# Optimization experiments

Measured on AMD Instinct MI355X. Metric: run time of the kernel, lower is better.

Reference implementation:

```python
import jax, jax.numpy as jnp
import numpy as np

N_EMBD = 1024
N_HEAD = 16
HEAD_DIM = N_EMBD // N_HEAD


def setup_inputs() -> dict:
    key = jax.random.key(0)
    kx, kq, kk, kv, ko = jax.random.split(key, 5)
    B, S = 2, 2048
    return {
        "x": jax.random.normal(kx, (B, S, N_EMBD), dtype=jnp.float32),
        "W_q": jax.random.normal(kq, (N_EMBD, N_EMBD), dtype=jnp.float32),
        "W_k": jax.random.normal(kk, (N_EMBD, N_EMBD), dtype=jnp.float32),
        "W_v": jax.random.normal(kv, (N_EMBD, N_EMBD), dtype=jnp.float32),
        "W_o": jax.random.normal(ko, (N_EMBD, N_EMBD), dtype=jnp.float32),
    }


def reference(x, W_q, W_k, W_v, W_o):
    B, S, E = x.shape
    H, D = N_HEAD, HEAD_DIM
    scale = 1.0 / np.sqrt(D).astype(np.float32)
    # QKV projections, split into heads: (B, H, S, D)
    q = (x @ W_q).reshape(B, S, H, D).transpose(0, 2, 1, 3)
    k = (x @ W_k).reshape(B, S, H, D).transpose(0, 2, 1, 3)
    v = (x @ W_v).reshape(B, S, H, D).transpose(0, 2, 1, 3)
    # scaled scores with causal mask
    scores = jnp.einsum("bhqd,bhkd->bhqk", q, k) * scale
    causal = jnp.tril(jnp.ones((S, S), dtype=bool))
    scores = jnp.where(causal, scores, -jnp.inf)
    attn = jax.nn.softmax(scores, axis=-1)
    out = jnp.einsum("bhqk,bhkd->bhqd", attn, v)
    out = out.transpose(0, 2, 1, 3).reshape(B, S, E)
    return out @ W_o
```

## Files before the change

### kernel.cpp

```cpp
#include <hip/hip_runtime.h>
#include <stdint.h>

#define E 1024
#define S 2048
#define NH 16
#define HD 64

typedef _Float16 f16;
typedef _Float16 f16x4 __attribute__((ext_vector_type(4)));
typedef _Float16 f16x8 __attribute__((ext_vector_type(8)));
typedef __fp16 hv4 __attribute__((ext_vector_type(4)));
typedef float f32x4 __attribute__((ext_vector_type(4)));

__device__ __forceinline__ void async16(const void* g, void* l) {
  __builtin_amdgcn_global_load_lds(
      (const __attribute__((address_space(1))) unsigned int*)g,
      (__attribute__((address_space(3))) unsigned int*)l, 16, 0, 0);
}


__global__ __launch_bounds__(256) void cvt_x(const float* __restrict__ x,
                                             f16* __restrict__ xh,
                                             f16* __restrict__ xl) {
  int i = (blockIdx.x * 256 + threadIdx.x) * 4;
  float4 a = *(const float4*)(x + i);
  f16 h0 = (f16)a.x, h1 = (f16)a.y, h2 = (f16)a.z, h3 = (f16)a.w;
  f16x4 hv = {h0, h1, h2, h3};
  f16x4 lv = {(f16)(a.x - (float)h0), (f16)(a.y - (float)h1),
              (f16)(a.z - (float)h2), (f16)(a.w - (float)h3)};
  *(f16x4*)(xh + i) = hv;
  *(f16x4*)(xl + i) = lv;
}

__global__ __launch_bounds__(256) void cvt_w(const float* __restrict__ Wq,
                                             const float* __restrict__ Wk,
                                             const float* __restrict__ Wv,
                                             const float* __restrict__ Wo,
                                             f16* __restrict__ Wh,
                                             f16* __restrict__ Wl) {
  __shared__ float tile[32][33];
  const int z = blockIdx.z;
  const float* W = z == 0 ? Wq : z == 1 ? Wk : z == 2 ? Wv : Wo;
  const int tx = threadIdx.x, ty = threadIdx.y;
  const int x0 = blockIdx.x * 32, y0 = blockIdx.y * 32;
#pragma unroll
  for (int i = 0; i < 4; i++)
    tile[ty + i * 8][tx] = W[(size_t)(y0 + ty + i * 8) * E + x0 + tx];
  __syncthreads();
  f16* outh = Wh + (size_t)z * E * E;
  f16* outl = Wl + (size_t)z * E * E;
#pragma unroll
  for (int i = 0; i < 4; i++) {
    float v = tile[tx][ty + i * 8];
    size_t o = (size_t)(x0 + ty + i * 8) * E + (y0 + tx);
    f16 hi = (f16)v;
    outh[o] = hi;
    if (z < 2) outl[o] = (f16)(v - (float)hi);
  }
}


template <bool SPLIT2>
__device__ __forceinline__ void gemm_mainloop(
    const f16* __restrict__ Ah, const f16* __restrict__ Al,
    const f16* __restrict__ Bh, const f16* __restrict__ Bl, int m0, int n0,
    int K, f16* Ahs, f16* Als, f16* Bhs, f16* Bls, f32x4 acc[4][4]) {
  const int tid = threadIdx.x, lane = tid & 63, wid = tid >> 6;
  const int quad = lane >> 4, c16 = lane & 15;
  const int rA = tid >> 2;
  const int cA = (tid & 3) ^ ((rA >> 1) & 3);
  const size_t gA0 = (size_t)(m0 + rA) * K + cA * 8;
  const size_t gA1 = (size_t)(m0 + 64 + rA) * K + cA * 8;
  const size_t gB0 = (size_t)(n0 + rA) * K + cA * 8;
  const size_t gB1 = (size_t)(n0 + 64 + rA) * K + cA * 8;
  const int l0 = tid * 8, l1 = (256 + tid) * 8;
  int a_off[4], b_off[4];
#pragma unroll
  for (int i = 0; i < 4; i++) {
    int ra = (wid >> 1) * 64 + i * 16 + c16;
    a_off[i] = ra * 32 + ((quad ^ ((ra >> 1) & 3)) << 3);
    int rb = (wid & 1) * 64 + i * 16 + c16;
    b_off[i] = rb * 32 + ((quad ^ ((rb >> 1) & 3)) << 3);
  }
  for (int k0 = 0; k0 < K; k0 += 32) {
    __syncthreads();
    async16(Ah + gA0 + k0, Ahs + l0);
    async16(Ah + gA1 + k0, Ahs + l1);
    async16(Bh + gB0 + k0, Bhs + l0);
    async16(Bh + gB1 + k0, Bhs + l1);
    if constexpr (SPLIT2) {
      async16(Al + gA0 + k0, Als + l0);
      async16(Al + gA1 + k0, Als + l1);
      async16(Bl + gB0 + k0, Bls + l0);
      async16(Bl + gB1 + k0, Bls + l1);
    }
    __syncthreads();
    f16x8 ah[4], bh[4];
#pragma unroll
    for (int i = 0; i < 4; i++) {
      ah[i] = *(const f16x8*)(Ahs + a_off[i]);
      bh[i] = *(const f16x8*)(Bhs + b_off[i]);
    }
    if constexpr (SPLIT2) {
      f16x8 al[4], bl[4];
#pragma unroll
      for (int i = 0; i < 4; i++) {
        al[i] = *(const f16x8*)(Als + a_off[i]);
        bl[i] = *(const f16x8*)(Bls + b_off[i]);
      }
#pragma unroll
      for (int i = 0; i < 4; i++)
#pragma unroll
        for (int j = 0; j < 4; j++) {
          acc[i][j] = __builtin_amdgcn_mfma_f32_16x16x32_f16(ah[i], bh[j], acc[i][j], 0, 0, 0);
          acc[i][j] = __builtin_amdgcn_mfma_f32_16x16x32_f16(ah[i], bl[j], acc[i][j], 0, 0, 0);
          acc[i][j] = __builtin_amdgcn_mfma_f32_16x16x32_f16(al[i], bh[j], acc[i][j], 0, 0, 0);
        }
    } else {
#pragma unroll
      for (int i = 0; i < 4; i++)
#pragma unroll
        for (int j = 0; j < 4; j++)
          acc[i][j] = __builtin_amdgcn_mfma_f32_16x16x32_f16(ah[i], bh[j], acc[i][j], 0, 0, 0);
    }
  }
}

__global__ __launch_bounds__(256) void qkv_gemm(
    const f16* __restrict__ xh, const f16* __restrict__ xl,
    const f16* __restrict__ Wh, const f16* __restrict__ Wl,
    f16* __restrict__ Qh, f16* __restrict__ Ql, f16* __restrict__ Kh,
    f16* __restrict__ Kl, f16* __restrict__ Vt) {
  __shared__ __align__(16) char smem_raw[36864];
  f16* Ahs = (f16*)smem_raw;
  f16* Als = Ahs + 4096;
  f16* Bhs = Ahs + 8192;
  f16* Bls = Ahs + 12288;
  const int z = blockIdx.z;
  const int m0 = blockIdx.y * 128, n0 = blockIdx.x * 128;
  const f16* Bth = Wh + (size_t)z * E * E;
  const f16* Btl = Wl + (size_t)z * E * E;
  f32x4 acc[4][4];
  const f32x4 zero4 = {0.f, 0.f, 0.f, 0.f};
#pragma unroll
  for (int i = 0; i < 4; i++)
#pragma unroll
    for (int j = 0; j < 4; j++) acc[i][j] = zero4;
  if (z < 2)
    gemm_mainloop<true>(xh, xl, Bth, Btl, m0, n0, E, Ahs, Als, Bhs, Bls, acc);
  else
    gemm_mainloop<false>(xh, nullptr, Bth, nullptr, m0, n0, E, Ahs, Als, Bhs, Bls, acc);
  const int tid = threadIdx.x, lane = tid & 63, wid = tid >> 6;
  const int quad = lane >> 4, c16 = lane & 15;
  if (z == 2) {
    __syncthreads();
    f16* vbuf = (f16*)smem_raw + (size_t)wid * 4608;
#pragma unroll
    for (int i = 0; i < 4; i++)
#pragma unroll
      for (int j = 0; j < 4; j++)
#pragma unroll
        for (int r = 0; r < 4; r++) {
          int sl = i * 16 + quad * 4 + r;
          int dl = j * 16 + c16;
          vbuf[dl * 72 + sl] = (f16)acc[i][j][r];
        }
#pragma unroll
    for (int i2 = 0; i2 < 8; i2++) {
      int dl = i2 * 8 + (lane >> 3);
      int ck = lane & 7;
      f16x8 v8 = *(const f16x8*)(vbuf + dl * 72 + ck * 8);
      int dg = n0 + (wid & 1) * 64 + dl;
      int sg = m0 + (wid >> 1) * 64 + ck * 8;
      int b = sg >> 11, s = sg & (S - 1);
      int h = dg >> 6, d = dg & 63;
      *(f16x8*)(Vt + (((size_t)(b * NH + h) * HD + d) << 11) + s) = v8;
    }
  } else {
#pragma unroll
    for (int i = 0; i < 4; i++)
#pragma unroll
      for (int j = 0; j < 4; j++)
#pragma unroll
        for (int r = 0; r < 4; r++) {
          int row = m0 + (wid >> 1) * 64 + i * 16 + quad * 4 + r;
          int col = n0 + (wid & 1) * 64 + j * 16 + c16;
          int b = row >> 11, s = row & (S - 1);
          int h = col >> 6, d = col & 63;
          float v = acc[i][j][r];
          size_t idx = (((size_t)(b * NH + h) * S + s) << 6) + d;
          f16 hi = (f16)v;
          f16 lo = (f16)(v - (float)hi);
          if (z == 0) { Qh[idx] = hi; Ql[idx] = lo; }
          else        { Kh[idx] = hi; Kl[idx] = lo; }
        }
  }
}

__global__ __launch_bounds__(256, 3) void flash(
    const f16* __restrict__ Qh, const f16* __restrict__ Ql,
    const f16* __restrict__ Kh, const f16* __restrict__ Kl,
    const f16* __restrict__ Vt, f16* __restrict__ Ao) {
  __shared__ __align__(16) f16 Khs[2][4096], Kls[2][4096], Vs[2][4096];
  const int tid = threadIdx.x, lane = tid & 63, wid = tid >> 6;
  const int quad = lane >> 4, c16 = lane & 15;
  const int flat = blockIdx.y * 16 + blockIdx.x;
  const int xcd = flat & 7, slot = flat >> 3;
  const int bh = xcd * 4 + (slot >> 4);
  const int qtile = 15 - (slot & 15);
  const int q0 = qtile * 128;
  const size_t bhoff = (size_t)bh * S * HD;
  const int qbase = wid * 32;
  f16x8 qf_h[2][2], qf_l[2][2];
#pragma unroll
  for (int qt = 0; qt < 2; qt++)
#pragma unroll
    for (int ks = 0; ks < 2; ks++) {
      int q = q0 + qbase + qt * 16 + c16;
      size_t off = bhoff + (size_t)q * HD + ks * 32 + quad * 8;
      qf_h[qt][ks] = *(const f16x8*)(Qh + off);
      qf_l[qt][ks] = *(const f16x8*)(Ql + off);
    }
  const int niter = 2 * qtile + 2;
  const int s0 = tid, s1 = 256 + tid;
  const int r0 = s0 >> 3, cc0 = ((s0 & 7) ^ (r0 & 7)) * 8;
  const int r1 = s1 >> 3, cc1 = ((s1 & 7) ^ (r1 & 7)) * 8;
  auto stage = [&](int it, int b) {
    const size_t kb = bhoff + (size_t)(it * 64) * HD;
    async16(Kh + kb + r0 * HD + cc0, &Khs[b][s0 * 8]);
    async16(Kh + kb + r1 * HD + cc1, &Khs[b][s1 * 8]);
    async16(Kl + kb + r0 * HD + cc0, &Kls[b][s0 * 8]);
    async16(Kl + kb + r1 * HD + cc1, &Kls[b][s1 * 8]);
    const size_t vb = bhoff + (size_t)(it * 64);
    async16(Vt + vb + (size_t)r0 * S + cc0, &Vs[b][s0 * 8]);
    async16(Vt + vb + (size_t)r1 * S + cc1, &Vs[b][s1 * 8]);
  };
  stage(0, 0);
  float mrow[2] = {-3.0e38f, -3.0e38f}, lsum[2] = {0.f, 0.f};
  f32x4 oacc[4][2];
  const f32x4 zero4 = {0.f, 0.f, 0.f, 0.f};
#pragma unroll
  for (int dt = 0; dt < 4; dt++)
#pragma unroll
    for (int qt = 0; qt < 2; qt++) oacc[dt][qt] = zero4;
  const int qrow0 = q0 + qbase + c16;
  const float cf = 0.18033688011112042f;
  for (int it = 0; it < niter; ++it) {
    const int cur = it & 1;
    __syncthreads();
    if (it + 1 < niter) stage(it + 1, cur ^ 1);
    const int k0 = it * 64;
    f32x4 st[2][4];
#pragma unroll
    for (int qt = 0; qt < 2; qt++)
#pragma unroll
      for (int kt = 0; kt < 4; kt++) st[qt][kt] = zero4;
#pragma unroll
    for (int kt = 0; kt < 4; kt++) {
      int rowk = (kt * 16 + c16) * 64;
      int sx = c16 & 7;
      f16x8 kh0 = *(const f16x8*)&Khs[cur][rowk + ((quad ^ sx) << 3)];
      f16x8 kh1 = *(const f16x8*)&Khs[cur][rowk + (((4 + quad) ^ sx) << 3)];
      f16x8 kl0 = *(const f16x8*)&Kls[cur][rowk + ((quad ^ sx) << 3)];
      f16x8 kl1 = *(const f16x8*)&Kls[cur][rowk + (((4 + quad) ^ sx) << 3)];
#pragma unroll
      for (int qt = 0; qt < 2; qt++) {
        st[qt][kt] = __builtin_amdgcn_mfma_f32_16x16x32_f16(kh0, qf_h[qt][0], st[qt][kt], 0, 0, 0);
        st[qt][kt] = __builtin_amdgcn_mfma_f32_16x16x32_f16(kh1, qf_h[qt][1], st[qt][kt], 0, 0, 0);
        st[qt][kt] = __builtin_amdgcn_mfma_f32_16x16x32_f16(kh0, qf_l[qt][0], st[qt][kt], 0, 0, 0);
        st[qt][kt] = __builtin_amdgcn_mfma_f32_16x16x32_f16(kh1, qf_l[qt][1], st[qt][kt], 0, 0, 0);
        st[qt][kt] = __builtin_amdgcn_mfma_f32_16x16x32_f16(kl0, qf_h[qt][0], st[qt][kt], 0, 0, 0);
        st[qt][kt] = __builtin_amdgcn_mfma_f32_16x16x32_f16(kl1, qf_h[qt][1], st[qt][kt], 0, 0, 0);
      }
    }
    const bool maskit = (it >= 2 * qtile);
    hv4 pb[2][4];
#pragma unroll
    for (int qt = 0; qt < 2; qt++) {
      const int qrow = qrow0 + qt * 16;
      if (maskit) {
#pragma unroll
        for (int kt = 0; kt < 4; kt++) {
          int kb = k0 + kt * 16 + quad * 4;
#pragma unroll
          for (int r = 0; r < 4; r++)
            if (kb + r > qrow) st[qt][kt][r] = -3.0e38f;
        }
      }
      float mx = -3.0e38f;
#pragma unroll
      for (int kt = 0; kt < 4; kt++) {
        float a = fmaxf(fmaxf(st[qt][kt][0], st[qt][kt][1]),
                        fmaxf(st[qt][kt][2], st[qt][kt][3]));
        mx = fmaxf(mx, a);
      }
      mx = fmaxf(mx, __shfl_xor(mx, 16, 64));
      mx = fmaxf(mx, __shfl_xor(mx, 32, 64));
      float mn = fmaxf(mrow[qt], mx);
      float alpha = __builtin_amdgcn_exp2f((mrow[qt] - mn) * cf);
      mrow[qt] = mn;
      float ls = lsum[qt] * alpha;
      float mncf = mn * cf;
#pragma unroll
      for (int kt = 0; kt < 4; kt++) {
        float p0 = __builtin_amdgcn_exp2f(st[qt][kt][0] * cf - mncf);
        float p1 = __builtin_amdgcn_exp2f(st[qt][kt][1] * cf - mncf);
        float p2 = __builtin_amdgcn_exp2f(st[qt][kt][2] * cf - mncf);
        float p3 = __builtin_amdgcn_exp2f(st[qt][kt][3] * cf - mncf);
        ls += (p0 + p1) + (p2 + p3);
        hv4 pv = {(__fp16)p0, (__fp16)p1, (__fp16)p2, (__fp16)p3};
        pb[qt][kt] = pv;
      }
      lsum[qt] = ls;
#pragma unroll
      for (int dt = 0; dt < 4; dt++) {
        oacc[dt][qt][0] *= alpha;
        oacc[dt][qt][1] *= alpha;
        oacc[dt][qt][2] *= alpha;
        oacc[dt][qt][3] *= alpha;
      }
    }
#pragma unroll
    for (int kt = 0; kt < 4; kt++) {
#pragma unroll
      for (int dt = 0; dt < 4; dt++) {
        int rowd = dt * 16 + c16;
        int cidx = (kt * 2 + (quad >> 1)) ^ (rowd & 7);
        hv4 vf = *(const hv4*)&Vs[cur][rowd * 64 + (cidx << 3) + (quad & 1) * 4];
#pragma unroll
        for (int qt = 0; qt < 2; qt++)
          oacc[dt][qt] = __builtin_amdgcn_mfma_f32_16x16x16f16(vf, pb[qt][kt], oacc[dt][qt], 0, 0, 0);
      }
    }
  }
  const int bb = bh >> 4, hh = bh & 15;
  float inv[2];
#pragma unroll
  for (int qt = 0; qt < 2; qt++) {
    float l = lsum[qt];
    l += __shfl_xor(l, 16, 64);
    l += __shfl_xor(l, 32, 64);
    inv[qt] = 1.0f / l;
  }
#pragma unroll
  for (int dt = 0; dt < 4; dt++)
#pragma unroll
    for (int qt = 0; qt < 2; qt++) {
      float iv = inv[qt];
      f16x4 ov = {(f16)(oacc[dt][qt][0] * iv), (f16)(oacc[dt][qt][1] * iv),
                  (f16)(oacc[dt][qt][2] * iv), (f16)(oacc[dt][qt][3] * iv)};
      int q = q0 + qbase + qt * 16 + c16;
      *(f16x4*)(Ao + ((size_t)(bb * S + q)) * E + hh * 64 + dt * 16 + quad * 4) = ov;
    }
}

__global__ __launch_bounds__(256) void out_gemm(const f16* __restrict__ Ao,
                                                const f16* __restrict__ Wo,
                                                float* __restrict__ Cout) {
  __shared__ __align__(16) f16 Ahs[4096], Bhs[4096];
  const int m0 = blockIdx.y * 128, n0 = blockIdx.x * 128;
  f32x4 acc[4][4];
  const f32x4 zero4 = {0.f, 0.f, 0.f, 0.f};
#pragma unroll
  for (int i = 0; i < 4; i++)
#pragma unroll
    for (int j = 0; j < 4; j++) acc[i][j] = zero4;
  gemm_mainloop<false>(Ao, nullptr, Wo, nullptr, m0, n0, E, Ahs, nullptr, Bhs, nullptr, acc);
  const int lane = threadIdx.x & 63, wid = threadIdx.x >> 6;
  const int quad = lane >> 4, c16 = lane & 15;
#pragma unroll
  for (int i = 0; i < 4; i++)
#pragma unroll
    for (int j = 0; j < 4; j++)
#pragma unroll
      for (int r = 0; r < 4; r++) {
        int row = m0 + (wid >> 1) * 64 + i * 16 + quad * 4 + r;
        int col = n0 + (wid & 1) * 64 + j * 16 + c16;
        Cout[(size_t)row * E + col] = acc[i][j][r];
      }
}

extern "C" void kernel_launch(void* const* d_in, const int* in_sizes, int n_in,
                              void* d_out, int out_size, void* d_ws,
                              size_t ws_size, hipStream_t stream) {
  const float* x = (const float*)d_in[0];
  const float* Wq = (const float*)d_in[1];
  const float* Wk = (const float*)d_in[2];
  const float* Wv = (const float*)d_in[3];
  const float* Wo = (const float*)d_in[4];
  char* ws = (char*)d_ws;
  const size_t MB = (size_t)1 << 20;
  f16* xh = (f16*)(ws + 0 * MB);
  f16* xl = (f16*)(ws + 8 * MB);
  f16* Wh = (f16*)(ws + 16 * MB);
  f16* Wl = (f16*)(ws + 24 * MB);
  f16* Qh = (f16*)(ws + 28 * MB);
  f16* Ql = (f16*)(ws + 36 * MB);
  f16* Kh = (f16*)(ws + 44 * MB);
  f16* Kl = (f16*)(ws + 52 * MB);
  f16* Vt = (f16*)(ws + 60 * MB);
  f16* Ao = (f16*)(ws + 68 * MB);
  cvt_x<<<4096, 256, 0, stream>>>(x, xh, xl);
  cvt_w<<<dim3(32, 32, 4), dim3(32, 8), 0, stream>>>(Wq, Wk, Wv, Wo, Wh, Wl);
  qkv_gemm<<<dim3(8, 32, 3), 256, 0, stream>>>(xh, xl, Wh, Wl, Qh, Ql, Kh, Kl, Vt);
  flash<<<dim3(16, 32), 256, 0, stream>>>(Qh, Ql, Kh, Kl, Vt, Ao);
  out_gemm<<<dim3(8, 32), 256, 0, stream>>>(Ao, Wh + (size_t)3 * E * E, (float*)d_out);
}
```

Baseline: 265.8 us.

## Shrink flash query tile to 64 rows, prescale Q/K, and coalesce Q/K stores

The flash kernel's query tile drops from 128 to 64 rows, so each wave handles 16 query rows. This doubles the grid to 1024 blocks, reduces per-block causal imbalance, and limits masking to the final diagonal iteration. The softmax scale times log2(e) is split as its square root and applied to both Q and K in the QKV epilogue, which removes a multiply from the inner exp. Q/K epilogue writes go through shared memory to produce 16-byte coalesced stores instead of scalar scattered stores. In exchange, K/V tiles are loaded from global memory twice as often per query row, and each block has half as many MFMAs per LDS read to hide latency.

```diff
diff --git a/kernel.cpp b/kernel.cpp
--- a/kernel.cpp
+++ b/kernel.cpp
@@ -152,9 +152,9 @@
     gemm_mainloop<false>(xh, nullptr, Bth, nullptr, m0, n0, E, Ahs, Als, Bhs, Bls, acc);
   const int tid = threadIdx.x, lane = tid & 63, wid = tid >> 6;
   const int quad = lane >> 4, c16 = lane & 15;
+  __syncthreads();
+  f16* vbuf = (f16*)smem_raw + (size_t)wid * 4608;
   if (z == 2) {
-    __syncthreads();
-    f16* vbuf = (f16*)smem_raw + (size_t)wid * 4608;
 #pragma unroll
     for (int i = 0; i < 4; i++)
 #pragma unroll
@@ -177,23 +177,35 @@
       *(f16x8*)(Vt + (((size_t)(b * NH + h) * HD + d) << 11) + s) = v8;
     }
   } else {
-#pragma unroll
-    for (int i = 0; i < 4; i++)
-#pragma unroll
-      for (int j = 0; j < 4; j++)
-#pragma unroll
-        for (int r = 0; r < 4; r++) {
-          int row = m0 + (wid >> 1) * 64 + i * 16 + quad * 4 + r;
-          int col = n0 + (wid & 1) * 64 + j * 16 + c16;
-          int b = row >> 11, s = row & (S - 1);
-          int h = col >> 6, d = col & 63;
-          float v = acc[i][j][r];
-          size_t idx = (((size_t)(b * NH + h) * S + s) << 6) + d;
-          f16 hi = (f16)v;
-          f16 lo = (f16)(v - (float)hi);
-          if (z == 0) { Qh[idx] = hi; Ql[idx] = lo; }
-          else        { Kh[idx] = hi; Kl[idx] = lo; }
-        }
+    const int t0 = m0 + (wid >> 1) * 64;
+    const int h = (n0 + (wid & 1) * 64) >> 6;
+    const float sc = 0.42466090014400953f;
+    f16* dsth = (z == 0) ? Qh : Kh;
+    f16* dstl = (z == 0) ? Ql : Kl;
+#pragma unroll
+    for (int pass = 0; pass < 2; pass++) {
+#pragma unroll
+      for (int i = 0; i < 4; i++)
+#pragma unroll
+        for (int j = 0; j < 4; j++)
+#pragma unroll
+          for (int r = 0; r < 4; r++) {
+            float v = acc[i][j][r] * sc;
+            f16 hi = (f16)v;
+            f16 outv = (pass == 0) ? hi : (f16)(v - (float)hi);
+            vbuf[(i * 16 + quad * 4 + r) * 72 + j * 16 + c16] = outv;
+          }
+      f16* dst = (pass == 0) ? dsth : dstl;
+#pragma unroll
+      for (int it = 0; it < 8; it++) {
+        int row = it * 8 + (lane >> 3);
+        int ck = lane & 7;
+        f16x8 v8 = *(const f16x8*)(vbuf + row * 72 + ck * 8);
+        int tok = t0 + row;
+        int b = tok >> 11, s = tok & (S - 1);
+        *(f16x8*)(dst + (((size_t)(b * NH + h) * S + s) << 6) + ck * 8) = v8;
+      }
+    }
   }
 }
 
@@ -204,24 +216,22 @@
   __shared__ __align__(16) f16 Khs[2][4096], Kls[2][4096], Vs[2][4096];
   const int tid = threadIdx.x, lane = tid & 63, wid = tid >> 6;
   const int quad = lane >> 4, c16 = lane & 15;
-  const int flat = blockIdx.y * 16 + blockIdx.x;
+  const int flat = blockIdx.y * 32 + blockIdx.x;
   const int xcd = flat & 7, slot = flat >> 3;
-  const int bh = xcd * 4 + (slot >> 4);
-  const int qtile = 15 - (slot & 15);
-  const int q0 = qtile * 128;
+  const int bh = xcd * 4 + (slot >> 5);
+  const int qtile = 31 - (slot & 31);
+  const int q0 = qtile * 64;
   const size_t bhoff = (size_t)bh * S * HD;
-  const int qbase = wid * 32;
-  f16x8 qf_h[2][2], qf_l[2][2];
-#pragma unroll
-  for (int qt = 0; qt < 2; qt++)
-#pragma unroll
-    for (int ks = 0; ks < 2; ks++) {
-      int q = q0 + qbase + qt * 16 + c16;
-      size_t off = bhoff + (size_t)q * HD + ks * 32 + quad * 8;
-      qf_h[qt][ks] = *(const f16x8*)(Qh + off);
-      qf_l[qt][ks] = *(const f16x8*)(Ql + off);
-    }
-  const int niter = 2 * qtile + 2;
+  const int qbase = wid * 16;
+  f16x8 qf_h[2], qf_l[2];
+#pragma unroll
+  for (int ks = 0; ks < 2; ks++) {
+    int q = q0 + qbase + c16;
+    size_t off = bhoff + (size_t)q * HD + ks * 32 + quad * 8;
+    qf_h[ks] = *(const f16x8*)(Qh + off);
+    qf_l[ks] = *(const f16x8*)(Ql + off);
+  }
+  const int niter = qtile + 1;
   const int s0 = tid, s1 = 256 + tid;
   const int r0 = s0 >> 3, cc0 = ((s0 & 7) ^ (r0 & 7)) * 8;
   const int r1 = s1 >> 3, cc1 = ((s1 & 7) ^ (r1 & 7)) * 8;
@@ -236,25 +246,20 @@
     async16(Vt + vb + (size_t)r1 * S + cc1, &Vs[b][s1 * 8]);
   };
   stage(0, 0);
-  float mrow[2] = {-3.0e38f, -3.0e38f}, lsum[2] = {0.f, 0.f};
-  f32x4 oacc[4][2];
+  float mrow = -3.0e38f, lsum = 0.f;
+  f32x4 oacc[4];
   const f32x4 zero4 = {0.f, 0.f, 0.f, 0.f};
 #pragma unroll
-  for (int dt = 0; dt < 4; dt++)
-#pragma unroll
-    for (int qt = 0; qt < 2; qt++) oacc[dt][qt] = zero4;
-  const int qrow0 = q0 + qbase + c16;
-  const float cf = 0.18033688011112042f;
+  for (int dt = 0; dt < 4; dt++) oacc[dt] = zero4;
+  const int qrow = q0 + qbase + c16;
   for (int it = 0; it < niter; ++it) {
     const int cur = it & 1;
     __syncthreads();
     if (it + 1 < niter) stage(it + 1, cur ^ 1);
     const int k0 = it * 64;
-    f32x4 st[2][4];
-#pragma unroll
-    for (int qt = 0; qt < 2; qt++)
-#pragma unroll
-      for (int kt = 0; kt < 4; kt++) st[qt][kt] = zero4;
+    f32x4 st[4];
+#pragma unroll
+    for (int kt = 0; kt < 4; kt++) st[kt] = zero4;
 #pragma unroll
     for (int kt = 0; kt < 4; kt++) {
       int rowk = (kt * 16 + c16) * 64;
@@ -263,62 +268,52 @@
       f16x8 kh1 = *(const f16x8*)&Khs[cur][rowk + (((4 + quad) ^ sx) << 3)];
       f16x8 kl0 = *(const f16x8*)&Kls[cur][rowk + ((quad ^ sx) << 3)];
       f16x8 kl1 = *(const f16x8*)&Kls[cur][rowk + (((4 + quad) ^ sx) << 3)];
-#pragma unroll
-      for (int qt = 0; qt < 2; qt++) {
-        st[qt][kt] = __builtin_amdgcn_mfma_f32_16x16x32_f16(kh0, qf_h[qt][0], st[qt][kt], 0, 0, 0);
-        st[qt][kt] = __builtin_amdgcn_mfma_f32_16x16x32_f16(kh1, qf_h[qt][1], st[qt][kt], 0, 0, 0);
-        st[qt][kt] = __builtin_amdgcn_mfma_f32_16x16x32_f16(kh0, qf_l[qt][0], st[qt][kt], 0, 0, 0);
-        st[qt][kt] = __builtin_amdgcn_mfma_f32_16x16x32_f16(kh1, qf_l[qt][1], st[qt][kt], 0, 0, 0);
-        st[qt][kt] = __builtin_amdgcn_mfma_f32_16x16x32_f16(kl0, qf_h[qt][0], st[qt][kt], 0, 0, 0);
-        st[qt][kt] = __builtin_amdgcn_mfma_f32_16x16x32_f16(kl1, qf_h[qt][1], st[qt][kt], 0, 0, 0);
-      }
-    }
-    const bool maskit = (it >= 2 * qtile);
-    hv4 pb[2][4];
-#pragma unroll
-    for (int qt = 0; qt < 2; qt++) {
-      const int qrow = qrow0 + qt * 16;
-      if (maskit) {
-#pragma unroll
-        for (int kt = 0; kt < 4; kt++) {
-          int kb = k0 + kt * 16 + quad * 4;
-#pragma unroll
-          for (int r = 0; r < 4; r++)
-            if (kb + r > qrow) st[qt][kt][r] = -3.0e38f;
-        }
-      }
-      float mx = -3.0e38f;
+      st[kt] = __builtin_amdgcn_mfma_f32_16x16x32_f16(kh0, qf_h[0], st[kt], 0, 0, 0);
+      st[kt] = __builtin_amdgcn_mfma_f32_16x16x32_f16(kh1, qf_h[1], st[kt], 0, 0, 0);
+      st[kt] = __builtin_amdgcn_mfma_f32_16x16x32_f16(kh0, qf_l[0], st[kt], 0, 0, 0);
+      st[kt] = __builtin_amdgcn_mfma_f32_16x16x32_f16(kh1, qf_l[1], st[kt], 0, 0, 0);
+      st[kt] = __builtin_amdgcn_mfma_f32_16x16x32_f16(kl0, qf_h[0], st[kt], 0, 0, 0);
+      st[kt] = __builtin_amdgcn_mfma_f32_16x16x32_f16(kl1, qf_h[1], st[kt], 0, 0, 0);
+    }
+    if (it == niter - 1) {
 #pragma unroll
       for (int kt = 0; kt < 4; kt++) {
-        float a = fmaxf(fmaxf(st[qt][kt][0], st[qt][kt][1]),
-                        fmaxf(st[qt][kt][2], st[qt][kt][3]));
-        mx = fmaxf(mx, a);
-      }
-      mx = fmaxf(mx, __shfl_xor(mx, 16, 64));
-      mx = fmaxf(mx, __shfl_xor(mx, 32, 64));
-      float mn = fmaxf(mrow[qt], mx);
-      float alpha = __builtin_amdgcn_exp2f((mrow[qt] - mn) * cf);
-      mrow[qt] = mn;
-      float ls = lsum[qt] * alpha;
-      float mncf = mn * cf;
-#pragma unroll
-      for (int kt = 0; kt < 4; kt++) {
-        float p0 = __builtin_amdgcn_exp2f(st[qt][kt][0] * cf - mncf);
-        float p1 = __builtin_amdgcn_exp2f(st[qt][kt][1] * cf - mncf);
-        float p2 = __builtin_amdgcn_exp2f(st[qt][kt][2] * cf - mncf);
-        float p3 = __builtin_amdgcn_exp2f(st[qt][kt][3] * cf - mncf);
-        ls += (p0 + p1) + (p2 + p3);
-        hv4 pv = {(__fp16)p0, (__fp16)p1, (__fp16)p2, (__fp16)p3};
-        pb[qt][kt] = pv;
-      }
-      lsum[qt] = ls;
-#pragma unroll
-      for (int dt = 0; dt < 4; dt++) {
-        oacc[dt][qt][0] *= alpha;
-        oacc[dt][qt][1] *= alpha;
-        oacc[dt][qt][2] *= alpha;
-        oacc[dt][qt][3] *= alpha;
-      }
+        int kb = k0 + kt * 16 + quad * 4;
+#pragma unroll
+        for (int r = 0; r < 4; r++)
+          if (kb + r > qrow) st[kt][r] = -3.0e38f;
+      }
+    }
+    float mx = -3.0e38f;
+#pragma unroll
+    for (int kt = 0; kt < 4; kt++) {
+      float a = fmaxf(fmaxf(st[kt][0], st[kt][1]), fmaxf(st[kt][2], st[kt][3]));
+      mx = fmaxf(mx, a);
+    }
+    mx = fmaxf(mx, __shfl_xor(mx, 16, 64));
+    mx = fmaxf(mx, __shfl_xor(mx, 32, 64));
+    float mn = fmaxf(mrow, mx);
+    float alpha = __builtin_amdgcn_exp2f(mrow - mn);
+    mrow = mn;
+    float ls = lsum * alpha;
+    hv4 pb[4];
+#pragma unroll
+    for (int kt = 0; kt < 4; kt++) {
+      float p0 = __builtin_amdgcn_exp2f(st[kt][0] - mn);
+      float p1 = __builtin_amdgcn_exp2f(st[kt][1] - mn);
+      float p2 = __builtin_amdgcn_exp2f(st[kt][2] - mn);
+      float p3 = __builtin_amdgcn_exp2f(st[kt][3] - mn);
+      ls += (p0 + p1) + (p2 + p3);
+      hv4 pv = {(__fp16)p0, (__fp16)p1, (__fp16)p2, (__fp16)p3};
+      pb[kt] = pv;
+    }
+    lsum = ls;
+#pragma unroll
+    for (int dt = 0; dt < 4; dt++) {
+      oacc[dt][0] *= alpha;
+      oacc[dt][1] *= alpha;
+      oacc[dt][2] *= alpha;
+      oacc[dt][3] *= alpha;
     }
 #pragma unroll
     for (int kt = 0; kt < 4; kt++) {
@@ -327,31 +322,22 @@
         int rowd = dt * 16 + c16;
         int cidx = (kt * 2 + (quad >> 1)) ^ (rowd & 7);
         hv4 vf = *(const hv4*)&Vs[cur][rowd * 64 + (cidx << 3) + (quad & 1) * 4];
-#pragma unroll
-        for (int qt = 0; qt < 2; qt++)
-          oacc[dt][qt] = __builtin_amdgcn_mfma_f32_16x16x16f16(vf, pb[qt][kt], oacc[dt][qt], 0, 0, 0);
+        oacc[dt] = __builtin_amdgcn_mfma_f32_16x16x16f16(vf, pb[kt], oacc[dt], 0, 0, 0);
       }
     }
   }
   const int bb = bh >> 4, hh = bh & 15;
-  float inv[2];
-#pragma unroll
-  for (int qt = 0; qt < 2; qt++) {
-    float l = lsum[qt];
-    l += __shfl_xor(l, 16, 64);
-    l += __shfl_xor(l, 32, 64);
-    inv[qt] = 1.0f / l;
-  }
-#pragma unroll
-  for (int dt = 0; dt < 4; dt++)
-#pragma unroll
-    for (int qt = 0; qt < 2; qt++) {
-      float iv = inv[qt];
-      f16x4 ov = {(f16)(oacc[dt][qt][0] * iv), (f16)(oacc[dt][qt][1] * iv),
-                  (f16)(oacc[dt][qt][2] * iv), (f16)(oacc[dt][qt][3] * iv)};
-      int q = q0 + qbase + qt * 16 + c16;
-      *(f16x4*)(Ao + ((size_t)(bb * S + q)) * E + hh * 64 + dt * 16 + quad * 4) = ov;
-    }
+  float l = lsum;
+  l += __shfl_xor(l, 16, 64);
+  l += __shfl_xor(l, 32, 64);
+  float iv = 1.0f / l;
+  const int q = q0 + qbase + c16;
+#pragma unroll
+  for (int dt = 0; dt < 4; dt++) {
+    f16x4 ov = {(f16)(oacc[dt][0] * iv), (f16)(oacc[dt][1] * iv),
+                (f16)(oacc[dt][2] * iv), (f16)(oacc[dt][3] * iv)};
+    *(f16x4*)(Ao + ((size_t)(bb * S + q)) * E + hh * 64 + dt * 16 + quad * 4) = ov;
+  }
 }
 
 __global__ __launch_bounds__(256) void out_gemm(const f16* __restrict__ Ao,
@@ -403,6 +389,6 @@
   cvt_x<<<4096, 256, 0, stream>>>(x, xh, xl);
   cvt_w<<<dim3(32, 32, 4), dim3(32, 8), 0, stream>>>(Wq, Wk, Wv, Wo, Wh, Wl);
   qkv_gemm<<<dim3(8, 32, 3), 256, 0, stream>>>(xh, xl, Wh, Wl, Qh, Ql, Kh, Kl, Vt);
-  flash<<<dim3(16, 32), 256, 0, stream>>>(Qh, Ql, Kh, Kl, Vt, Ao);
+  flash<<<dim3(32, 32), 256, 0, stream>>>(Qh, Ql, Kh, Kl, Vt, Ao);
   out_gemm<<<dim3(8, 32), 256, 0, stream>>>(Ao, Wh + (size_t)3 * E * E, (float*)d_out);
 }
```

Measured after the change: 276.3 us. 1.04x slower.
